# Optimization experiments

Hardware: AMD Instinct MI355X
Metric: run time of the kernel (lower is better)

The kernel has to match this reference:

```python
import jax, jax.numpy as jnp
import numpy as np

GROUPS = 32
EPS = 1e-5


def setup_inputs() -> dict:
    key = jax.random.key(0)
    ks = jax.random.split(key, 4)
    B, C, H, W = 16, 512, 32, 32
    x = jax.random.normal(ks[0], (B, C, H, W), dtype=jnp.float32)
    gamma = jnp.ones((C,), jnp.float32)
    beta = jnp.zeros((C,), jnp.float32)
    # 1x1 convs as channel GEMMs; fan-in scaled init
    w_qkv = jax.random.normal(ks[1], (3 * C, C), dtype=jnp.float32) / np.sqrt(C)
    b_qkv = jnp.zeros((3 * C,), jnp.float32)
    w_proj = jax.random.normal(ks[2], (C, C), dtype=jnp.float32) / np.sqrt(C)
    b_proj = jnp.zeros((C,), jnp.float32)
    return {"x": x, "gamma": gamma, "beta": beta, "w_qkv": w_qkv,
            "b_qkv": b_qkv, "w_proj": w_proj, "b_proj": b_proj}


def _group_norm(x, gamma, beta):
    B, C, H, W = x.shape
    xg = x.reshape(B, GROUPS, C // GROUPS, H, W)
    mu = xg.mean(axis=(2, 3, 4), keepdims=True)
    var = xg.var(axis=(2, 3, 4), keepdims=True)
    xn = ((xg - mu) * jax.lax.rsqrt(var + EPS)).reshape(B, C, H, W)
    return xn * gamma[None, :, None, None] + beta[None, :, None, None]


def reference(x, gamma, beta, w_qkv, b_qkv, w_proj, b_proj):
    B, C, H, W = x.shape
    xn = _group_norm(x, gamma, beta)
    # 1x1 conv qkv: [B, 3C, H, W]
    qkv = jnp.einsum('oc,bchw->bohw', w_qkv, xn) + b_qkv[None, :, None, None]
    qkv = qkv.reshape(B, 3, C, H * W)
    q, k, v = qkv[:, 0], qkv[:, 1], qkv[:, 2]  # each [B, C, HW]
    scale = C ** (-0.5)
    # attn[b, i, j] = softmax_j( q[b,:,i] . k[b,:,j] * scale )
    attn = jax.nn.softmax(jnp.einsum('bci,bcj->bij', q, k) * scale, axis=-1)
    # out[b, c, i] = sum_j v[b,c,j] * attn[b,i,j]
    out = jnp.einsum('bcj,bij->bci', v, attn).reshape(B, C, H, W)
    proj = jnp.einsum('oc,bchw->bohw', w_proj, out) + b_proj[None, :, None, None]
    return x + proj
```

## Files before the change

kernel.cpp:

```cpp
#include <hip/hip_runtime.h>


typedef _Float16 f16;
typedef _Float16 f16x8 __attribute__((ext_vector_type(8)));
typedef _Float16 f16x4 __attribute__((ext_vector_type(4)));
typedef float fx4 __attribute__((ext_vector_type(4)));

__device__ __forceinline__ void gload16(const f16* g, f16* l) {
    __builtin_amdgcn_global_load_lds((const __attribute__((address_space(1))) void*)g,
                                     (__attribute__((address_space(3))) void*)l, 16, 0, 0);
}

__global__ __launch_bounds__(256)
void wconv_kernel(const float* __restrict__ w, f16* __restrict__ o, int n4)
{
    int i = blockIdx.x * 256 + threadIdx.x;
    if (i < n4) {
        float4 v = *(const float4*)(w + i * 4);
        f16x4 h;
        h[0] = (f16)v.x; h[1] = (f16)v.y; h[2] = (f16)v.z; h[3] = (f16)v.w;
        *(f16x4*)(o + i * 4) = h;
    }
}

__global__ __launch_bounds__(256)
void groupnorm_kernel(const float* __restrict__ x, const float* __restrict__ gamma,
                      const float* __restrict__ beta, f16* __restrict__ xnT)
{
    __shared__ float red[256], red2[256];
    __shared__ float mu_s, rs_s;
    __shared__ __align__(16) f16 T[16][1040];
    const int blk = blockIdx.x;
    const int b = blk >> 5, g = blk & 31;
    const long base = (long)blk * 16384;
    const int tid = threadIdx.x;
    const float4* xv = (const float4*)(x + base);

    float4 xr[16];
    float s = 0.f, s2 = 0.f;
#pragma unroll
    for (int i = 0; i < 16; i++) {
        float4 v = xv[tid + i * 256];
        xr[i] = v;
        s  += v.x + v.y + v.z + v.w;
        s2 += v.x * v.x + v.y * v.y + v.z * v.z + v.w * v.w;
    }
    red[tid] = s; red2[tid] = s2;
    __syncthreads();
    for (int off = 128; off > 0; off >>= 1) {
        if (tid < off) { red[tid] += red[tid + off]; red2[tid] += red2[tid + off]; }
        __syncthreads();
    }
    if (tid == 0) {
        float mu = red[0] * (1.f / 16384.f);
        float var = red2[0] * (1.f / 16384.f) - mu * mu;
        mu_s = mu;
        rs_s = rsqrtf(var + 1e-5f);
    }
    __syncthreads();
    const float mu = mu_s, rs = rs_s;

#pragma unroll
    for (int i = 0; i < 16; i++) {
        float gm = gamma[g * 16 + i] * rs;
        float bt = beta[g * 16 + i] - mu * gm;
        float4 v = xr[i];
        f16x4 o;
        o[0] = (f16)(v.x * gm + bt);
        o[1] = (f16)(v.y * gm + bt);
        o[2] = (f16)(v.z * gm + bt);
        o[3] = (f16)(v.w * gm + bt);
        *(f16x4*)&T[i][tid * 4] = o;
    }
    __syncthreads();
#pragma unroll
    for (int i = 0; i < 8; i++) {
        int idx = tid + i * 256;
        int hw = idx >> 1;
        int half8 = (idx & 1) * 8;
        f16x8 o;
#pragma unroll
        for (int j = 0; j < 8; j++) o[j] = T[half8 + j][hw];
        long dst = ((long)b * 1024 + hw) * 512 + g * 16 + half8;
        *(f16x8*)(xnT + dst) = o;
    }
}

__global__ __launch_bounds__(256)
void softmax_kernel(f16* __restrict__ S)
{
    const int wid = blockIdx.x * 4 + (threadIdx.x >> 6);
    const int lane = threadIdx.x & 63;
    f16* p = S + (long)wid * 1024 + lane * 16;
    f16x8 h0 = *(const f16x8*)p;
    f16x8 h1 = *(const f16x8*)(p + 8);
    float v[16];
#pragma unroll
    for (int i = 0; i < 8; i++) { v[i] = (float)h0[i]; v[8 + i] = (float)h1[i]; }
    float mx = v[0];
#pragma unroll
    for (int i = 1; i < 16; i++) mx = fmaxf(mx, v[i]);
    for (int off = 32; off > 0; off >>= 1) mx = fmaxf(mx, __shfl_xor(mx, off, 64));
    float sum = 0.f;
#pragma unroll
    for (int i = 0; i < 16; i++) { v[i] = __expf(v[i] - mx); sum += v[i]; }
    for (int off = 32; off > 0; off >>= 1) sum += __shfl_xor(sum, off, 64);
    const float inv = 1.f / sum;
#pragma unroll
    for (int i = 0; i < 8; i++) { h0[i] = (f16)(v[i] * inv); h1[i] = (f16)(v[8 + i] * inv); }
    *(f16x8*)p = h0;
    *(f16x8*)(p + 8) = h1;
}

template<int MODE>
__global__ __launch_bounds__(256)
void gemm_kernel(const f16* __restrict__ Ap, const f16* __restrict__ Bp,
                 void* __restrict__ Cp, f16* __restrict__ C2p,
                 const float* __restrict__ bias, const float* __restrict__ resid,
                 float alpha, int M, int N, int K, int lda, int ldb,
                 long sAb, long sBb, long sCb)
{
    __shared__ __align__(16) f16 As[2][128 * 32];
    __shared__ __align__(16) f16 Bs[2][128 * 32];

    const int linear = (blockIdx.z * gridDim.y + blockIdx.y) * gridDim.x + blockIdx.x;
    const int nTiles = gridDim.x, nm = gridDim.x * gridDim.y;
    const int x7 = linear & 7, slot = linear >> 3;
    const int b = x7 + 8 * (slot / nm);
    const int rem = slot % nm;
    const int mIdx = rem / nTiles, nIdx = rem % nTiles;
    const int m0 = mIdx * 128, n0 = nIdx * 128;

    const int tid = threadIdx.x;
    const int wave = tid >> 6, lane = tid & 63;
    const int quad = lane >> 4, l15 = lane & 15;
    const int wm = (wave >> 1) * 64, wn = (wave & 1) * 64;
    const int chunkoff = (quad ^ ((l15 >> 1) & 3)) * 8;

    const f16* Ag = Ap + (long)b * sAb;
    const f16* Bg = Bp + (long)b * sBb;

    const int si = lane >> 2, sj = lane & 3;
    const int swz = (sj ^ ((si >> 1) & 3)) * 8;
    const int R = wave * 32;
    const f16* agA = Ag + (long)(m0 + R + si) * lda + swz;
    const f16* agB = Bg + (long)(n0 + R + si) * ldb + swz;

    fx4 acc[4][4] = {};
    const int nIter = K >> 5;

#define STAGE(buf, kOff)                                              \
    { gload16(agA + (kOff),            &As[buf][R * 32]);             \
      gload16(agA + 16 * lda + (kOff), &As[buf][(R + 16) * 32]);      \
      gload16(agB + (kOff),            &Bs[buf][R * 32]);             \
      gload16(agB + 16 * ldb + (kOff), &Bs[buf][(R + 16) * 32]); }

    STAGE(0, 0)

    for (int it = 0; it < nIter; ++it) {
        __syncthreads();
        const int cur = it & 1;
        if (it + 1 < nIter) { STAGE(cur ^ 1, (it + 1) << 5) }
        f16x8 bf[4];
#pragma unroll
        for (int tn = 0; tn < 4; tn++)
            bf[tn] = *(const f16x8*)&Bs[cur][(wn + tn * 16 + l15) * 32 + chunkoff];
#pragma unroll
        for (int tm = 0; tm < 4; tm++) {
            f16x8 af = *(const f16x8*)&As[cur][(wm + tm * 16 + l15) * 32 + chunkoff];
#pragma unroll
            for (int tn = 0; tn < 4; tn++)
                acc[tm][tn] = __builtin_amdgcn_mfma_f32_16x16x32_f16(af, bf[tn], acc[tm][tn], 0, 0, 0);
        }
    }
#undef STAGE

    if (MODE == 1 && n0 >= 1024) {
#pragma unroll
        for (int tm = 0; tm < 4; tm++)
#pragma unroll
        for (int tn = 0; tn < 4; tn++) {
            int gc = n0 + wn + tn * 16 + l15;
            int gr0 = m0 + wm + tm * 16 + quad * 4;
            float bs = bias[gc];
            f16x4 o;
#pragma unroll
            for (int r = 0; r < 4; r++) o[r] = (f16)(acc[tm][tn][r] + bs);
            *(f16x4*)(C2p + (long)b * 524288 + (long)(gc - 1024) * 1024 + gr0) = o;
        }
        return;
    }
#pragma unroll
    for (int tm = 0; tm < 4; tm++)
#pragma unroll
    for (int tn = 0; tn < 4; tn++) {
        int gc = n0 + wn + tn * 16 + l15;
#pragma unroll
        for (int r = 0; r < 4; r++) {
            int gr = m0 + wm + tm * 16 + quad * 4 + r;
            float v = acc[tm][tn][r];
            if (MODE == 0) {
                v *= alpha;
                ((f16*)Cp)[(long)b * sCb + (long)gr * N + gc] = (f16)v;
            } else if (MODE == 1) {
                v += bias[gc];
                ((f16*)Cp)[(long)b * 1048576 + (long)gr * 1024 + gc] = (f16)v;
            } else {
                v += bias[gr];
                long idx = (long)b * sCb + (long)gr * N + gc;
                v += resid[idx];
                ((float*)Cp)[idx] = v;
            }
        }
    }
}

extern "C" void kernel_launch(void* const* d_in, const int* in_sizes, int n_in,
                              void* d_out, int out_size, void* d_ws, size_t ws_size,
                              hipStream_t stream)
{
    const float* x      = (const float*)d_in[0];
    const float* gamma  = (const float*)d_in[1];
    const float* beta   = (const float*)d_in[2];
    const float* w_qkv  = (const float*)d_in[3];
    const float* b_qkv  = (const float*)d_in[4];
    const float* w_proj = (const float*)d_in[5];
    const float* b_proj = (const float*)d_in[6];
    float* out = (float*)d_out;

    char* ws = (char*)d_ws;
    f16* xnT   = (f16*)(ws);
    f16* qkT   = (f16*)(ws + (16L << 20));
    f16* vbuf  = (f16*)(ws + (48L << 20));
    f16* S     = (f16*)(ws + (64L << 20));
    f16* aoutT = (f16*)(ws + (96L << 20));
    f16* wqkvh = S;
    f16* wprjh = xnT;

    wconv_kernel<<<768, 256, 0, stream>>>(w_qkv, wqkvh, 196608);

    groupnorm_kernel<<<512, 256, 0, stream>>>(x, gamma, beta, xnT);

    gemm_kernel<1><<<dim3(12, 8, 16), 256, 0, stream>>>(
        xnT, wqkvh, qkT, vbuf, b_qkv, nullptr, 1.0f,
        1024, 1536, 512, 512, 512,
        524288L, 0L, 0L);

    wconv_kernel<<<256, 256, 0, stream>>>(w_proj, wprjh, 65536);

    gemm_kernel<0><<<dim3(8, 8, 16), 256, 0, stream>>>(
        qkT, qkT + 512, S, nullptr, nullptr, nullptr, 0.04419417382415922f,
        1024, 1024, 512, 1024, 1024,
        1048576L, 1048576L, 1048576L);

    softmax_kernel<<<4096, 256, 0, stream>>>(S);

    gemm_kernel<0><<<dim3(4, 8, 16), 256, 0, stream>>>(
        S, vbuf, aoutT, nullptr, nullptr, nullptr, 1.0f,
        1024, 512, 1024, 1024, 1024,
        1048576L, 524288L, 524288L);

    gemm_kernel<2><<<dim3(8, 4, 16), 256, 0, stream>>>(
        wprjh, aoutT, out, nullptr, b_proj, x, 1.0f,
        512, 1024, 512, 512, 512,
        0L, 524288L, 524288L);
}
```

Baseline: 235.9 us.

## Replace GEMM with persistent 256x128-tile kernel using 4-stage LDS pipeline

The batched GEMM kernel becomes persistent: 256 blocks of 512 threads loop over tiles in an XCD-aware order. Each tile grows to 256x128 and uses a 4-buffer LDS ring with prefetch two steps ahead. The MFMA work is split into two halves separated by barriers, with s_setprio raised around the MFMAs so loads and math interleave. The goal is to cut launch and tail overhead, improve data reuse and hide global-load latency. The cost is more LDS, more hand-placed waitcnt and barrier ordering that could be fragile, and fewer blocks resident per CU.

```diff
diff --git a/kernel.cpp b/kernel.cpp
--- a/kernel.cpp
+++ b/kernel.cpp
@@ -113,23 +113,18 @@
 }
 
 template<int MODE>
-__global__ __launch_bounds__(256)
-void gemm_kernel(const f16* __restrict__ Ap, const f16* __restrict__ Bp,
-                 void* __restrict__ Cp, f16* __restrict__ C2p,
-                 const float* __restrict__ bias, const float* __restrict__ resid,
-                 float alpha, int M, int N, int K, int lda, int ldb,
-                 long sAb, long sBb, long sCb)
-{
-    __shared__ __align__(16) f16 As[2][128 * 32];
-    __shared__ __align__(16) f16 Bs[2][128 * 32];
-
-    const int linear = (blockIdx.z * gridDim.y + blockIdx.y) * gridDim.x + blockIdx.x;
-    const int nTiles = gridDim.x, nm = gridDim.x * gridDim.y;
-    const int x7 = linear & 7, slot = linear >> 3;
-    const int b = x7 + 8 * (slot / nm);
-    const int rem = slot % nm;
-    const int mIdx = rem / nTiles, nIdx = rem % nTiles;
-    const int m0 = mIdx * 128, n0 = nIdx * 128;
+__global__ __launch_bounds__(512, 2)
+void pgemm_kernel(const f16* __restrict__ Ap, const f16* __restrict__ Bp,
+                  void* __restrict__ Cp, f16* __restrict__ C2p,
+                  const float* __restrict__ bias, const float* __restrict__ resid,
+                  float alpha, int K, int lda, int ldb, int N,
+                  int nm, int tpb, int nT,
+                  long sAb, long sBb, long sCb)
+{
+    __shared__ __align__(16) f16 As[4][256 * 32];
+    __shared__ __align__(16) f16 Bs[4][128 * 32];
+
+    const int blk = (blockIdx.x & 7) * 32 + (blockIdx.x >> 3);
 
     const int tid = threadIdx.x;
     const int wave = tid >> 6, lane = tid & 63;
@@ -137,79 +132,106 @@
     const int wm = (wave >> 1) * 64, wn = (wave & 1) * 64;
     const int chunkoff = (quad ^ ((l15 >> 1) & 3)) * 8;
 
-    const f16* Ag = Ap + (long)b * sAb;
-    const f16* Bg = Bp + (long)b * sBb;
-
-    const int si = lane >> 2, sj = lane & 3;
-    const int swz = (sj ^ ((si >> 1) & 3)) * 8;
-    const int R = wave * 32;
-    const f16* agA = Ag + (long)(m0 + R + si) * lda + swz;
-    const f16* agB = Bg + (long)(n0 + R + si) * ldb + swz;
-
-    fx4 acc[4][4] = {};
-    const int nIter = K >> 5;
-
-#define STAGE(buf, kOff)                                              \
-    { gload16(agA + (kOff),            &As[buf][R * 32]);             \
-      gload16(agA + 16 * lda + (kOff), &As[buf][(R + 16) * 32]);      \
-      gload16(agB + (kOff),            &Bs[buf][R * 32]);             \
-      gload16(agB + 16 * ldb + (kOff), &Bs[buf][(R + 16) * 32]); }
-
-    STAGE(0, 0)
-
-    for (int it = 0; it < nIter; ++it) {
-        __syncthreads();
-        const int cur = it & 1;
-        if (it + 1 < nIter) { STAGE(cur ^ 1, (it + 1) << 5) }
-        f16x8 bf[4];
-#pragma unroll
-        for (int tn = 0; tn < 4; tn++)
-            bf[tn] = *(const f16x8*)&Bs[cur][(wn + tn * 16 + l15) * 32 + chunkoff];
-#pragma unroll
-        for (int tm = 0; tm < 4; tm++) {
-            f16x8 af = *(const f16x8*)&As[cur][(wm + tm * 16 + l15) * 32 + chunkoff];
-#pragma unroll
-            for (int tn = 0; tn < 4; tn++)
-                acc[tm][tn] = __builtin_amdgcn_mfma_f32_16x16x32_f16(af, bf[tn], acc[tm][tn], 0, 0, 0);
+    const int rl = lane >> 2;
+    const int swzc = ((lane & 3) ^ ((rl >> 1) & 3)) * 8;
+    const int RA = wave * 32;
+    const int RB = wave * 16;
+    const int H = K >> 5;
+
+    for (int id = blk; id < nT; id += 256) {
+        const int b  = id / tpb, r = id % tpb;
+        const int m0 = (r % nm) * 256, n0 = (r / nm) * 128;
+        const f16* agA = Ap + (long)b * sAb + (long)(m0 + RA + rl) * lda + swzc;
+        const f16* agB = Bp + (long)b * sBb + (long)(n0 + RB + rl) * ldb + swzc;
+
+        gload16(agA,                 &As[0][RA * 32]);
+        gload16(agA + 16 * lda,      &As[0][(RA + 16) * 32]);
+        gload16(agB,                 &Bs[0][RB * 32]);
+        gload16(agA + 32,            &As[1][RA * 32]);
+        gload16(agA + 16 * lda + 32, &As[1][(RA + 16) * 32]);
+        gload16(agB + 32,            &Bs[1][RB * 32]);
+        asm volatile("s_waitcnt vmcnt(3)" ::: "memory");
+        __builtin_amdgcn_s_barrier();
+
+        fx4 acc[4][4] = {};
+        for (int s = 0; s < H; ++s) {
+            const f16* Ab = &As[s & 3][0];
+            const f16* Bb = &Bs[s & 3][0];
+            const bool pre = (s + 2 < H);
+            f16x8 af[4], bf[4];
+#pragma unroll
+            for (int fm = 0; fm < 4; fm++)
+                af[fm] = *(const f16x8*)&Ab[(wm + fm * 16 + l15) * 32 + chunkoff];
+#pragma unroll
+            for (int fn = 0; fn < 2; fn++)
+                bf[fn] = *(const f16x8*)&Bb[(wn + fn * 16 + l15) * 32 + chunkoff];
+            if (pre) {
+                f16* d = &As[(s + 2) & 3][0];
+                gload16(agA + (long)(s + 2) * 32,            d + RA * 32);
+                gload16(agA + 16 * lda + (long)(s + 2) * 32, d + (RA + 16) * 32);
+            }
+            __builtin_amdgcn_s_barrier();
+            __builtin_amdgcn_s_setprio(1);
+#pragma unroll
+            for (int fm = 0; fm < 4; fm++)
+#pragma unroll
+                for (int fn = 0; fn < 2; fn++)
+                    acc[fm][fn] = __builtin_amdgcn_mfma_f32_16x16x32_f16(af[fm], bf[fn], acc[fm][fn], 0, 0, 0);
+            __builtin_amdgcn_s_setprio(0);
+            __builtin_amdgcn_s_barrier();
+#pragma unroll
+            for (int fn = 2; fn < 4; fn++)
+                bf[fn] = *(const f16x8*)&Bb[(wn + fn * 16 + l15) * 32 + chunkoff];
+            if (pre)
+                gload16(agB + (long)(s + 2) * 32, &Bs[(s + 2) & 3][RB * 32]);
+            __builtin_amdgcn_s_setprio(1);
+#pragma unroll
+            for (int fm = 0; fm < 4; fm++)
+#pragma unroll
+                for (int fn = 2; fn < 4; fn++)
+                    acc[fm][fn] = __builtin_amdgcn_mfma_f32_16x16x32_f16(af[fm], bf[fn], acc[fm][fn], 0, 0, 0);
+            __builtin_amdgcn_s_setprio(0);
+            if (pre)               { asm volatile("s_waitcnt vmcnt(3)" ::: "memory"); }
+            else if (s == H - 2)   { asm volatile("s_waitcnt vmcnt(0)" ::: "memory"); }
+            __builtin_amdgcn_s_barrier();
         }
-    }
-#undef STAGE
-
-    if (MODE == 1 && n0 >= 1024) {
-#pragma unroll
-        for (int tm = 0; tm < 4; tm++)
-#pragma unroll
-        for (int tn = 0; tn < 4; tn++) {
-            int gc = n0 + wn + tn * 16 + l15;
-            int gr0 = m0 + wm + tm * 16 + quad * 4;
-            float bs = bias[gc];
-            f16x4 o;
-#pragma unroll
-            for (int r = 0; r < 4; r++) o[r] = (f16)(acc[tm][tn][r] + bs);
-            *(f16x4*)(C2p + (long)b * 524288 + (long)(gc - 1024) * 1024 + gr0) = o;
-        }
-        return;
-    }
-#pragma unroll
-    for (int tm = 0; tm < 4; tm++)
-#pragma unroll
-    for (int tn = 0; tn < 4; tn++) {
-        int gc = n0 + wn + tn * 16 + l15;
-#pragma unroll
-        for (int r = 0; r < 4; r++) {
-            int gr = m0 + wm + tm * 16 + quad * 4 + r;
-            float v = acc[tm][tn][r];
-            if (MODE == 0) {
-                v *= alpha;
-                ((f16*)Cp)[(long)b * sCb + (long)gr * N + gc] = (f16)v;
-            } else if (MODE == 1) {
-                v += bias[gc];
-                ((f16*)Cp)[(long)b * 1048576 + (long)gr * 1024 + gc] = (f16)v;
-            } else {
-                v += bias[gr];
-                long idx = (long)b * sCb + (long)gr * N + gc;
-                v += resid[idx];
-                ((float*)Cp)[idx] = v;
+
+        if (MODE == 1 && n0 >= 1024) {
+#pragma unroll
+            for (int tm = 0; tm < 4; tm++)
+#pragma unroll
+            for (int tn = 0; tn < 4; tn++) {
+                int gc = n0 + wn + tn * 16 + l15;
+                int gr0 = m0 + wm + tm * 16 + quad * 4;
+                float bs = bias[gc];
+                f16x4 o;
+#pragma unroll
+                for (int rr = 0; rr < 4; rr++) o[rr] = (f16)(acc[tm][tn][rr] + bs);
+                *(f16x4*)(C2p + (long)b * 524288 + (long)(gc - 1024) * 1024 + gr0) = o;
+            }
+        } else {
+#pragma unroll
+            for (int tm = 0; tm < 4; tm++)
+#pragma unroll
+            for (int tn = 0; tn < 4; tn++) {
+                int gc = n0 + wn + tn * 16 + l15;
+#pragma unroll
+                for (int rr = 0; rr < 4; rr++) {
+                    int gr = m0 + wm + tm * 16 + quad * 4 + rr;
+                    float v = acc[tm][tn][rr];
+                    if (MODE == 0) {
+                        v *= alpha;
+                        ((f16*)Cp)[(long)b * sCb + (long)gr * N + gc] = (f16)v;
+                    } else if (MODE == 1) {
+                        v += bias[gc];
+                        ((f16*)Cp)[(long)b * 1048576 + (long)gr * 1024 + gc] = (f16)v;
+                    } else {
+                        v += bias[gr];
+                        long idx = (long)b * sCb + (long)gr * N + gc;
+                        v += resid[idx];
+                        ((float*)Cp)[idx] = v;
+                    }
+                }
             }
         }
     }
@@ -241,27 +263,31 @@
 
     groupnorm_kernel<<<512, 256, 0, stream>>>(x, gamma, beta, xnT);
 
-    gemm_kernel<1><<<dim3(12, 8, 16), 256, 0, stream>>>(
+    pgemm_kernel<1><<<256, 512, 0, stream>>>(
         xnT, wqkvh, qkT, vbuf, b_qkv, nullptr, 1.0f,
-        1024, 1536, 512, 512, 512,
+        512, 512, 512, 1536,
+        4, 48, 768,
         524288L, 0L, 0L);
 
     wconv_kernel<<<256, 256, 0, stream>>>(w_proj, wprjh, 65536);
 
-    gemm_kernel<0><<<dim3(8, 8, 16), 256, 0, stream>>>(
+    pgemm_kernel<0><<<256, 512, 0, stream>>>(
         qkT, qkT + 512, S, nullptr, nullptr, nullptr, 0.04419417382415922f,
-        1024, 1024, 512, 1024, 1024,
+        512, 1024, 1024, 1024,
+        4, 32, 512,
         1048576L, 1048576L, 1048576L);
 
     softmax_kernel<<<4096, 256, 0, stream>>>(S);
 
-    gemm_kernel<0><<<dim3(4, 8, 16), 256, 0, stream>>>(
+    pgemm_kernel<0><<<256, 512, 0, stream>>>(
         S, vbuf, aoutT, nullptr, nullptr, nullptr, 1.0f,
-        1024, 512, 1024, 1024, 1024,
+        1024, 1024, 1024, 512,
+        4, 16, 256,
         1048576L, 524288L, 524288L);
 
-    gemm_kernel<2><<<dim3(8, 4, 16), 256, 0, stream>>>(
+    pgemm_kernel<2><<<256, 512, 0, stream>>>(
         wprjh, aoutT, out, nullptr, b_proj, x, 1.0f,
-        512, 1024, 512, 512, 512,
+        512, 512, 512, 1024,
+        2, 16, 256,
         0L, 524288L, 524288L);
 }
```

Measured after the change: 230.0 us. -2.5%, faster.
